# Kernel tuning notes

Hardware: AMD Instinct MI355X
Metric: run time of the kernel (lower is better)

The kernel has to match this reference:

```python
import jax, jax.numpy as jnp
from jax import lax
import numpy as np

L, G, C = 4, 2, 4  # num_blocks, num_sparsity_groups, num_sparsity_cardinals
IMAGE_MEAN = 0.5
SCALE = 2


def _wn(v, g):
    # weight_norm over dims (1,2,3), g per output channel
    n = jnp.sqrt(jnp.sum(v * v, axis=(1, 2, 3), keepdims=True))
    return (g.reshape(-1, 1, 1, 1) / n) * v


def _conv(x, w, b, pad):
    y = lax.conv_general_dilated(x, w, (1, 1), [(pad, pad), (pad, pad)],
                                 dimension_numbers=('NCHW', 'OIHW', 'NCHW'))
    return y + b[None, :, None, None]


def _dyn_conv(x, v, g, b, mw, mb):
    # sparsity-routed conv: per-sample expert mixture of kernels
    w = _wn(v, g)                                   # [G*out, in, k, k]
    B = x.shape[0]
    logits = x.mean((-1, -2)) @ mw.T + mb           # [B, G*C]
    s = jax.nn.softmax(logits.reshape(B, G, C), axis=1)
    wv = w.reshape(G, C, -1, *w.shape[1:])          # [G, C, D, in, k, k]
    wper = jnp.einsum('bgc,gcdikl->bcdikl', s, wv)
    wper = wper.reshape(B, -1, *w.shape[1:])        # [B, out, in, k, k]
    bper = jnp.einsum('bgc,gcd->bcd', s, b.reshape(G, C, -1)).reshape(B, -1)

    def per_sample(xi, wi, bi):
        yi = lax.conv_general_dilated(xi[None], wi, (1, 1), [(1, 1), (1, 1)],
                                      dimension_numbers=('NCHW', 'OIHW', 'NCHW'))[0]
        return yi + bi[:, None, None]

    return jax.vmap(per_sample)(x, wper, bper)


def _pixel_shuffle(x, r):
    B, Cc, H, W = x.shape
    x = x.reshape(B, Cc // (r * r), r, r, H, W)
    x = x.transpose(0, 1, 4, 2, 5, 3)
    return x.reshape(B, Cc // (r * r), H * r, W * r)


def setup_inputs() -> dict:
    key = jax.random.key(0)
    ks = jax.random.split(key, 16)
    f32 = jnp.float32
    inp = {
        'x': jax.random.uniform(ks[0], (8, 3, 64, 64), dtype=f32),
        'head_v': jax.random.normal(ks[1], (64, 3, 3, 3), dtype=f32) * 0.05,
        'head_g': jnp.ones((64,), f32),
        'head_b': jnp.zeros((64,), f32),
        'b1_v': jax.random.normal(ks[2], (L, 512, 64, 3, 3), dtype=f32) * 0.05,
        'b1_g': jnp.full((L, 512), 2.0, f32),
        'b1_b': jnp.zeros((L, 512), f32),
        'b1_mw': jax.random.normal(ks[3], (L, 8, 64), dtype=f32) * 0.05,
        'b1_mb': jax.random.normal(ks[4], (L, 8), dtype=f32) * 0.05,
        'b2_v': jax.random.normal(ks[5], (L, 128, 256, 3, 3), dtype=f32) * 0.05,
        'b2_g': jnp.full((L, 128), 1.0 / np.sqrt(L), f32),
        'b2_b': jnp.zeros((L, 128), f32),
        'b2_mw': jax.random.normal(ks[6], (L, 8, 256), dtype=f32) * 0.05,
        'b2_mb': jax.random.normal(ks[7], (L, 8), dtype=f32) * 0.05,
        'tail_v': jax.random.normal(ks[8], (12, 64, 3, 3), dtype=f32) * 0.05,
        'tail_g': jnp.ones((12,), f32),
        'tail_b': jnp.zeros((12,), f32),
        'skip_v': jax.random.normal(ks[9], (12, 3, 5, 5), dtype=f32) * 0.05,
        'skip_g': jnp.ones((12,), f32),
        'skip_b': jnp.zeros((12,), f32),
    }
    return inp


def reference(x, head_v, head_g, head_b,
              b1_v, b1_g, b1_b, b1_mw, b1_mb,
              b2_v, b2_g, b2_b, b2_mw, b2_mb,
              tail_v, tail_g, tail_b,
              skip_v, skip_g, skip_b):
    x = x - IMAGE_MEAN
    h = _conv(x, _wn(head_v, head_g), head_b, pad=1)
    for l in range(L):
        r0 = h
        t = _dyn_conv(h, b1_v[l], b1_g[l], b1_b[l], b1_mw[l], b1_mb[l])
        t = jax.nn.relu(t)
        t = _dyn_conv(t, b2_v[l], b2_g[l], b2_b[l], b2_mw[l], b2_mb[l])
        h = t + r0
    body = _conv(h, _wn(tail_v, tail_g), tail_b, pad=1)
    s = _conv(x, _wn(skip_v, skip_g), skip_b, pad=2)
    y = _pixel_shuffle(body + s, SCALE) + IMAGE_MEAN
    return y
```

## Files before the change

kernel.cpp:

```cpp
#include <hip/hip_runtime.h>

typedef __attribute__((ext_vector_type(8))) short bf16x8;
typedef __attribute__((ext_vector_type(4))) float f32x4;
typedef __attribute__((ext_vector_type(8))) unsigned short u16x8;

__device__ __forceinline__ unsigned short bf16u(float x) {
    unsigned int u = __builtin_bit_cast(unsigned int, x);
    unsigned int r = (u + 0x7fffu + ((u >> 16) & 1u)) >> 16;
    return (unsigned short)r;
}
__device__ __forceinline__ float bf2f(unsigned short u) {
    return __builtin_bit_cast(float, (unsigned int)u << 16);
}
__device__ __forceinline__ void gll16(const void* g, void* l) {
    __builtin_amdgcn_global_load_lds((const __attribute__((address_space(1))) void*)g,
                                     (__attribute__((address_space(3))) void*)l, 16, 0, 0);
}

__global__ __launch_bounds__(256) void setup_kernel(
    unsigned short* __restrict__ hbf, unsigned short* __restrict__ tbf,
    float* __restrict__ sums,
    const float* __restrict__ hv, const float* __restrict__ hg, float* __restrict__ hw,
    const float* __restrict__ kv, const float* __restrict__ kg, float* __restrict__ kw) {
    int blk = blockIdx.x;
    if (blk < 335) {
        int i = blk * 256 + threadIdx.x;
        u16x8 z8 = {0, 0, 0, 0, 0, 0, 0, 0};
        if (i < 16640) {
            int chv = i & 3, pb = i >> 2, pos = pb % 260, bc = pb / 260;
            int y, x;
            if (pos < 66) { y = 0; x = pos; }
            else if (pos < 132) { y = 65; x = pos - 66; }
            else if (pos < 196) { y = pos - 131; x = 0; }
            else { y = pos - 195; x = 65; }
            *(u16x8*)&hbf[((size_t)bc * 4356 + y * 66 + x) * 32 + chv * 8] = z8;
        } else if (i < 83200) {
            int j = i - 16640;
            int chv = j & 3, pb = j >> 2, pos = pb % 260, bc = pb / 260;
            int y, x;
            if (pos < 66) { y = 0; x = pos; }
            else if (pos < 132) { y = 65; x = pos - 66; }
            else if (pos < 196) { y = pos - 131; x = 0; }
            else { y = pos - 195; x = 65; }
            *(u16x8*)&tbf[((size_t)bc * 4356 + y * 66 + x) * 32 + chv * 8] = z8;
        } else {
            int k = i - 83200;
            f32x4 z4 = {0.f, 0.f, 0.f, 0.f};
            ((f32x4*)sums)[k] = z4;
        }
        return;
    }
    int b2 = blk - 335;
    const float *v, *g;
    float* outw;
    int len, row;
    if (b2 < 64) { v = hv; g = hg; outw = hw; len = 27; row = b2; }
    else         { v = kv; g = kg; outw = kw; len = 75; row = b2 - 64; }
    __shared__ float red[4];
    __shared__ float s_sc;
    const float* vr = v + (size_t)row * len;
    float ss = 0.f;
    for (int i = threadIdx.x; i < len; i += 256) { float a = vr[i]; ss += a * a; }
    for (int o = 32; o > 0; o >>= 1) ss += __shfl_down(ss, o);
    if ((threadIdx.x & 63) == 0) red[threadIdx.x >> 6] = ss;
    __syncthreads();
    if (threadIdx.x == 0) s_sc = g[row] / sqrtf(red[0] + red[1] + red[2] + red[3]);
    __syncthreads();
    float sc = s_sc;
    float* orow = outw + (size_t)row * len;
    for (int i = threadIdx.x; i < len; i += 256) orow[i] = vr[i] * sc;
}

__global__ __launch_bounds__(256) void tail_repack2(const float* __restrict__ tv,
                                                    const float* __restrict__ tg,
                                                    unsigned short* __restrict__ wq) {
    __shared__ float row[576];
    __shared__ float red[4];
    __shared__ float s_sc;
    int mo = blockIdx.x;
    int tid = threadIdx.x;
    if (mo < 12) {
        for (int i = tid; i < 576; i += 256) row[i] = tv[mo * 576 + i];
        __syncthreads();
        float ss = 0.f;
        for (int i = tid; i < 576; i += 256) { float a = row[i]; ss += a * a; }
        for (int o = 32; o > 0; o >>= 1) ss += __shfl_down(ss, o);
        if ((tid & 63) == 0) red[tid >> 6] = ss;
        __syncthreads();
        if (tid == 0) s_sc = tg[mo] / sqrtf(red[0] + red[1] + red[2] + red[3]);
        __syncthreads();
        float sc = s_sc;
        for (int ch = tid; ch < 72; ch += 256) {
            int kg = ch & 3, c2 = ch >> 2;
            int t = c2 % 9, kc = c2 / 9;
            u16x8 pk;
#pragma unroll
            for (int kj = 0; kj < 8; ++kj) {
                int ic = kc * 32 + kg * 8 + kj;
                pk[kj] = bf16u(row[ic * 9 + t] * sc);
            }
            *(u16x8*)&wq[(size_t)((kc * 9 + t) * 4 + kg) * 128 + mo * 8] = pk;
        }
    } else {
        u16x8 z = {0, 0, 0, 0, 0, 0, 0, 0};
        for (int ch = tid; ch < 72; ch += 256) {
            int kg = ch & 3, c2 = ch >> 2;
            int t = c2 % 9, kc = c2 / 9;
            *(u16x8*)&wq[(size_t)((kc * 9 + t) * 4 + kg) * 128 + mo * 8] = z;
        }
    }
}

template <int IC, int GOC, int BPB, int LGMO>
__global__ __launch_bounds__(256) void combine_v3(
    const float* __restrict__ v, const float* __restrict__ g,
    const float* __restrict__ msum, const float* __restrict__ mw,
    const float* __restrict__ mb, float* __restrict__ s_out,
    unsigned short* __restrict__ wq, int D, int OC) {
    constexpr int ROWF = IC * 9;
    constexpr int KCh = IC / 32;
    constexpr int ROWS2 = 2 * GOC;
    constexpr int TOTC = GOC * KCh * 9 * 4;
    __shared__ float lv[ROWS2 * ROWF];
    __shared__ float lg[BPB][8];
    __shared__ float sv[BPB][8];
    __shared__ float scr[ROWS2];
    __shared__ float sw[BPB][ROWS2];
    int tid = threadIdx.x;
    int ocg = blockIdx.x * GOC;
    int b0 = blockIdx.y * BPB;
    for (int i = tid; i < ROWS2 * ROWF; i += 256) {
        int r = i / ROWF, jj = i - r * ROWF;
        int oc_r = (r / GOC) * OC + ocg + (r % GOC);
        lv[i] = v[(size_t)oc_r * ROWF + jj];
    }
    {
        int j = tid >> 5, l32 = tid & 31;
        for (int bb = 0; bb < BPB; ++bb) {
            float part = 0.f;
            for (int i = l32; i < IC; i += 32) part += msum[(b0 + bb) * IC + i] * mw[j * IC + i];
            for (int m = 16; m > 0; m >>= 1) part += __shfl_xor(part, m);
            if (l32 == 0) lg[bb][j] = part * (1.f / 4096.f) + mb[j];
        }
    }
    __syncthreads();
    {
        constexpr int TPR = 256 / ROWS2;
        int r = tid / TPR, lr = tid % TPR;
        float ss = 0.f;
        for (int i = lr; i < ROWF; i += TPR) { float a = lv[r * ROWF + i]; ss += a * a; }
#pragma unroll
        for (int m = (TPR > 32 ? 32 : TPR / 2); m > 0; m >>= 1) ss += __shfl_xor(ss, m);
        if (lr == 0) {
            int oc_r = (r / GOC) * OC + ocg + (r % GOC);
            scr[r] = g[oc_r] / sqrtf(ss);
        }
    }
    if (tid < BPB * 8) {
        int bb = tid >> 3, j = tid & 7;
        int gg = j >> 2, c = j & 3;
        float l0 = lg[bb][c], l1 = lg[bb][4 + c];
        float m = fmaxf(l0, l1);
        float e0 = __expf(l0 - m), e1 = __expf(l1 - m);
        float val = ((gg == 0) ? e0 : e1) / (e0 + e1);
        sv[bb][j] = val;
        if (blockIdx.x == 0) s_out[(b0 + bb) * 8 + j] = val;
    }
    __syncthreads();
    if (tid < BPB * ROWS2) {
        int bb = tid / ROWS2, r = tid % ROWS2;
        int oc = ocg + (r % GOC);
        int cd = oc / D;
        float s = (r < GOC) ? sv[bb][cd] : sv[bb][4 + cd];
        sw[bb][r] = s * scr[r];
    }
    __syncthreads();
    for (int ci = tid; ci < TOTC; ci += 256) {
        int ml = ci % GOC;
        int c = ci / GOC;
        int kg = c & 3, c2 = c >> 2;
        int t = c2 % 9, kc = c2 / 9;
        int oc = ocg + ml;
        const float* p0 = &lv[(size_t)ml * ROWF];
        const float* p1 = &lv[(size_t)(GOC + ml) * ROWF];
        float a0[8], a1[8];
#pragma unroll
        for (int kj = 0; kj < 8; ++kj) {
            int ic9 = (kc * 32 + kg * 8 + kj) * 9 + t;
            a0[kj] = p0[ic9];
            a1[kj] = p1[ic9];
        }
        for (int bb = 0; bb < BPB; ++bb) {
            float s0 = sw[bb][ml], s1 = sw[bb][GOC + ml];
            u16x8 pk;
#pragma unroll
            for (int kj = 0; kj < 8; ++kj) pk[kj] = bf16u(s0 * a0[kj] + s1 * a1[kj]);
            int b = b0 + bb;
            size_t w_off = ((((size_t)(b * (OC >> LGMO) + (oc >> LGMO)) * KCh + kc) * 9 + t) * 4 + kg)
                               * ((1 << LGMO) * 8) + (size_t)(oc & ((1 << LGMO) - 1)) * 8;
            *(u16x8*)&wq[w_off] = pk;
        }
    }
}

template <int IC, int OC, int MT, int WM, int WN, int NR,
          bool RELU, bool RES, bool WF32, bool WBF, int OCR, bool DYNB, int MINW>
__global__ __launch_bounds__(WM * WN * 64, MINW)
void conv_mfma(
    const unsigned short* __restrict__ in_bf,
    const unsigned short* __restrict__ wq,
    const float* __restrict__ bias_raw, const float* __restrict__ s8, int lgD,
    float* __restrict__ out,
    unsigned short* __restrict__ out_bf, float* __restrict__ msum, long wstride) {
    constexpr int THREADS = WM * WN * 64;
    constexpr int KCH = IC / 32;
    constexpr int NRH = NR + 2;
    constexpr int NT = NR * 64;
    constexpr int NF = (NT / 16) / WN;
    constexpr int MW = MT / (16 * WM);
    constexpr int WELEM = 9 * 32 * MT;
    constexpr int SELEM = NRH * 66 * 32;
    constexpr int SCH = SELEM / 8;
    constexpr int OCB = OCR / 32;

    __shared__ __align__(16) unsigned short S[2][SELEM];
    __shared__ float MRED[WN][MT];

    const int b = blockIdx.x, ot = blockIdx.z;
    const int y0 = blockIdx.y * NR;
    const int tid = threadIdx.x;
    const int lane = tid & 63;
    const int wid = tid >> 6;
    const int wm = wid / WN, wn = wid % WN;
    const int l15 = lane & 15, lk = lane >> 4;
    const int wmo = wm * (MT / WM);
    const int wno = wn * (NT / WN);

    f32x4 acc[MW][NF];
#pragma unroll
    for (int mf = 0; mf < MW; ++mf)
#pragma unroll
        for (int nf = 0; nf < NF; ++nf)
#pragma unroll
            for (int q = 0; q < 4; ++q) acc[mf][nf][q] = 0.f;

    const unsigned short* inb = in_bf + (size_t)b * KCH * (4356 * 32);
    const unsigned short* wqb = wq + (size_t)b * wstride + (size_t)ot * (KCH * WELEM);
    const unsigned short* wqa = wqb + (size_t)lk * (MT * 8) + (size_t)(wmo + l15) * 8;

    auto STAGE_S = [&](int kc, int buf) {
        const unsigned short* sb = inb + (size_t)kc * (4356 * 32);
        for (int i = tid; i < SCH; i += THREADS) {
            int Lz = i ^ ((i >> 3) & 7);
            int lk2 = Lz & 3, cr = Lz >> 2;
            int col = cr % 66, row = cr / 66;
            gll16(sb + ((size_t)(y0 + row) * 66 + col) * 32 + lk2 * 8,
                  (char*)S[buf] + i * 16);
        }
    };

    bf16x8 aT[2][MW];
#pragma unroll
    for (int mf = 0; mf < MW; ++mf) {
        aT[0][mf] = *(const bf16x8*)(wqa + mf * 128);
        aT[1][mf] = *(const bf16x8*)(wqa + (4 * MT * 8) + mf * 128);
    }
    STAGE_S(0, 0);
    __syncthreads();
#pragma unroll
    for (int kc = 0; kc < KCH; ++kc) {
        if (kc + 1 < KCH) STAGE_S(kc + 1, (kc + 1) & 1);
        const unsigned short* Sb = S[kc & 1];
#pragma unroll
        for (int t = 0; t < 9; ++t) {
            const int gt = kc * 9 + t;
            const int pp = gt & 1;
            const int dy = t / 3, dx = t % 3;
#pragma unroll
            for (int nf = 0; nf < NF; ++nf) {
                int n = wno + nf * 16 + l15;
                int r = n >> 6, c = n & 63;
                int L = ((r + dy) * 66 + (c + dx)) * 4 + lk;
                int P = L ^ ((L >> 3) & 7);
                bf16x8 bv = *(const bf16x8*)((const char*)Sb + P * 16);
#pragma unroll
                for (int mf = 0; mf < MW; ++mf)
                    acc[mf][nf] = __builtin_amdgcn_mfma_f32_16x16x32_bf16(aT[pp][mf], bv, acc[mf][nf], 0, 0, 0);
            }
            if (gt + 2 < KCH * 9) {
                const int ngt = gt + 2;
                const int nkc = ngt / 9, nt2 = ngt % 9;
#pragma unroll
                for (int mf = 0; mf < MW; ++mf)
                    aT[pp][mf] = *(const bf16x8*)(wqa + (size_t)nkc * WELEM + nt2 * (4 * MT * 8) + mf * 128);
            }
        }
        __syncthreads();
    }

    if constexpr (WBF) {
        static_assert(NF == 2, "shuffle epilogue needs NF==2");
        const int mynf = lk & 1;
        const int ch = lk >> 1;
        const bool evenlk = ((lk & 1) == 0);
#pragma unroll
        for (int mf = 0; mf < MW; ++mf) {
            int ocb = ot * MT + wmo + mf * 16 + lk * 4;
            float bvv[4];
#pragma unroll
            for (int q = 0; q < 4; ++q) {
                int oc = ocb + q;
                if (DYNB) {
                    int cc = oc >> lgD;
                    bvv[q] = s8[b * 8 + cc] * bias_raw[oc] + s8[b * 8 + 4 + cc] * bias_raw[OCR + oc];
                } else {
                    bvv[q] = bias_raw[oc];
                }
            }
            float r[2][4], pr[2][4];
#pragma unroll
            for (int nf = 0; nf < 2; ++nf)
#pragma unroll
                for (int q = 0; q < 4; ++q) {
                    float v = acc[mf][nf][q] + bvv[q];
                    if (RELU) v = fmaxf(v, 0.f);
                    r[nf][q] = v;
                }
#pragma unroll
            for (int nf = 0; nf < 2; ++nf)
#pragma unroll
                for (int q = 0; q < 4; ++q) pr[nf][q] = __shfl_xor(r[nf][q], 16);
            float v8[8];
#pragma unroll
            for (int q = 0; q < 4; ++q) {
                float a = r[mynf][q], p = pr[mynf][q];
                v8[q] = evenlk ? a : p;
                v8[4 + q] = evenlk ? p : a;
            }
            int n = wno + mynf * 16 + l15;
            int y = y0 + (n >> 6), x = n & 63;
            int occ = ot * MT + wmo + mf * 16 + ch * 8;
            size_t addr = ((((size_t)b * OCB + (occ >> 5)) * 66 + (y + 1)) * 66 + (x + 1)) * 32
                          + (occ & 31);
            if (RES) {
                u16x8 rv = *(const u16x8*)&out_bf[addr];
#pragma unroll
                for (int j = 0; j < 8; ++j) v8[j] += bf2f(rv[j]);
            }
            u16x8 pk;
#pragma unroll
            for (int j = 0; j < 8; ++j) pk[j] = bf16u(v8[j]);
            *(u16x8*)&out_bf[addr] = pk;
            if (msum) {
#pragma unroll
                for (int j = 0; j < 8; ++j) {
                    float t = v8[j];
                    t += __shfl_xor(t, 1);
                    t += __shfl_xor(t, 2);
                    t += __shfl_xor(t, 4);
                    t += __shfl_xor(t, 8);
                    t += __shfl_xor(t, 16);
                    v8[j] = t;
                }
                if ((lane & 31) == 0) {
#pragma unroll
                    for (int j = 0; j < 8; ++j)
                        MRED[wn][wmo + mf * 16 + ch * 8 + j] = v8[j];
                }
            }
        }
        if (msum) {
            __syncthreads();
            if (tid < MT) {
                float tot = 0.f;
#pragma unroll
                for (int w2 = 0; w2 < WN; ++w2) tot += MRED[w2][tid];
                atomicAdd(&msum[b * OCR + ot * MT + tid], tot);
            }
        }
    }
    if constexpr (WF32) {
#pragma unroll
        for (int mf = 0; mf < MW; ++mf) {
            int ocb = ot * MT + wmo + mf * 16 + lk * 4;
#pragma unroll
            for (int nf = 0; nf < NF; ++nf) {
                int n = wno + nf * 16 + l15;
                int y = y0 + (n >> 6), x = n & 63;
#pragma unroll
                for (int q = 0; q < 4; ++q) {
                    int oc = ocb + q;
                    if (oc < OCR) {
                        float v = acc[mf][nf][q] + bias_raw[oc];
                        out[(((size_t)b * OCR + oc) * 64 + y) * 64 + x] = v;
                    }
                }
            }
        }
    }
}

__global__ __launch_bounds__(256) void head_conv(
    const float* __restrict__ in, const float* __restrict__ w,
    const float* __restrict__ bias,
    unsigned short* __restrict__ out_bf, float* __restrict__ hsum0) {
    constexpr int OCT = 16, IC = 3;
    __shared__ float s_in[34 * 34];
    __shared__ float s_w[OCT * 9];
    __shared__ float wred[4][OCT];
    int b = blockIdx.z;
    int ocBase = blockIdx.y * OCT;
    int ty0 = (blockIdx.x >> 1) * 32;
    int tx0 = (blockIdx.x & 1) * 32;
    int tid = threadIdx.x;
    int lane = tid & 63, wid = tid >> 6;
    int tx = tid & 15, ty = tid >> 4;

    float acc[OCT][4];
#pragma unroll
    for (int oc = 0; oc < OCT; ++oc)
#pragma unroll
        for (int p = 0; p < 4; ++p) acc[oc][p] = 0.f;

    const float* inb = in + (size_t)b * IC * 4096;
    for (int ic = 0; ic < IC; ++ic) {
        const float* src = inb + (size_t)ic * 4096;
        for (int i = tid; i < 34 * 34; i += 256) {
            int r = i / 34, cc = i % 34;
            int gy = ty0 + r - 1, gx = tx0 + cc - 1;
            float val = 0.f;
            if (gy >= 0 && gy < 64 && gx >= 0 && gx < 64) val = src[gy * 64 + gx] - 0.5f;
            s_in[i] = val;
        }
        for (int i = tid; i < OCT * 9; i += 256) {
            int oc = i / 9, t = i % 9;
            s_w[i] = w[((size_t)(ocBase + oc) * IC + ic) * 9 + t];
        }
        __syncthreads();
        float v[4][4];
#pragma unroll
        for (int r = 0; r < 4; ++r)
#pragma unroll
            for (int cc = 0; cc < 4; ++cc) v[r][cc] = s_in[(2 * ty + r) * 34 + (2 * tx + cc)];
#pragma unroll
        for (int oc = 0; oc < OCT; ++oc) {
#pragma unroll
            for (int ky = 0; ky < 3; ++ky)
#pragma unroll
                for (int kx = 0; kx < 3; ++kx) {
                    float wv = s_w[oc * 9 + ky * 3 + kx];
                    acc[oc][0] += wv * v[ky][kx];
                    acc[oc][1] += wv * v[ky][kx + 1];
                    acc[oc][2] += wv * v[ky + 1][kx];
                    acc[oc][3] += wv * v[ky + 1][kx + 1];
                }
        }
        __syncthreads();
    }
    int py = ty0 + 2 * ty, px = tx0 + 2 * tx;
#pragma unroll
    for (int oc = 0; oc < OCT; ++oc) {
        int og = ocBase + oc;
        float bv = bias[og];
        float osum = 0.f;
#pragma unroll
        for (int p = 0; p < 4; ++p) {
            int dy = p >> 1, dx = p & 1;
            float val = acc[oc][p] + bv;
            osum += val;
            out_bf[((size_t)(b * 2 + (og >> 5)) * 4356 + (py + dy + 1) * 66 + (px + dx + 1)) * 32
                   + (og & 31)] = bf16u(val);
        }
        for (int m = 1; m < 64; m <<= 1) osum += __shfl_xor(osum, m);
        if (lane == 0) wred[wid][oc] = osum;
    }
    __syncthreads();
    if (tid < OCT)
        atomicAdd(&hsum0[b * 64 + ocBase + tid],
                  wred[0][tid] + wred[1][tid] + wred[2][tid] + wred[3][tid]);
}

__global__ __launch_bounds__(256) void shuffle_skip(
    const float* __restrict__ body, const float* __restrict__ x,
    const float* __restrict__ skw, const float* __restrict__ skb,
    float* __restrict__ out) {
    __shared__ float w[900];
    __shared__ float bb[12];
    int tid = threadIdx.x;
    for (int i = tid; i < 900; i += 256) w[i] = skw[i];
    if (tid < 12) bb[tid] = skb[tid];
    __syncthreads();
    int idx = blockIdx.x * 256 + tid;
    int ox = idx & 127;
    int oy = (idx >> 7) & 127;
    int v = idx >> 14;
    int c = v % 3;
    int b = v / 3;
    int rx = ox & 1, ry = oy & 1;
    int xx = ox >> 1, yy = oy >> 1;
    int ch = c * 4 + ry * 2 + rx;
    float acc = bb[ch];
    for (int ic = 0; ic < 3; ++ic)
        for (int ky = 0; ky < 5; ++ky) {
            int gy = yy + ky - 2;
            if (gy < 0 || gy >= 64) continue;
            for (int kx = 0; kx < 5; ++kx) {
                int gx = xx + kx - 2;
                if (gx < 0 || gx >= 64) continue;
                acc += w[((ch * 3 + ic) * 5 + ky) * 5 + kx] *
                       (x[((size_t)(b * 3 + ic) * 64 + gy) * 64 + gx] - 0.5f);
            }
        }
    size_t src = (((size_t)b * 12 + ch) * 64 + yy) * 64 + xx;
    out[idx] = body[src] + acc + 0.5f;
}

extern "C" void kernel_launch(void* const* d_in, const int* in_sizes, int n_in,
                              void* d_out, int out_size, void* d_ws, size_t ws_size,
                              hipStream_t stream) {
    const float* x      = (const float*)d_in[0];
    const float* head_v = (const float*)d_in[1];
    const float* head_g = (const float*)d_in[2];
    const float* head_b = (const float*)d_in[3];
    const float* b1_v   = (const float*)d_in[4];
    const float* b1_g   = (const float*)d_in[5];
    const float* b1_b   = (const float*)d_in[6];
    const float* b1_mw  = (const float*)d_in[7];
    const float* b1_mb  = (const float*)d_in[8];
    const float* b2_v   = (const float*)d_in[9];
    const float* b2_g   = (const float*)d_in[10];
    const float* b2_b   = (const float*)d_in[11];
    const float* b2_mw  = (const float*)d_in[12];
    const float* b2_mb  = (const float*)d_in[13];
    const float* tail_v = (const float*)d_in[14];
    const float* tail_g = (const float*)d_in[15];
    const float* tail_b = (const float*)d_in[16];
    const float* skip_v = (const float*)d_in[17];
    const float* skip_g = (const float*)d_in[18];
    const float* skip_b = (const float*)d_in[19];

    float* ws = (float*)d_ws;
    size_t off = 0;
    auto alloc = [&](size_t n) { float* p = ws + off; off += (n + 3) & ~(size_t)3; return p; };
    float* head_w = alloc(64 * 27);
    float* skip_w = alloc(12 * 75);
    float* sums   = alloc(10240);
    float* sbuf   = alloc(64);
    float* body   = alloc((size_t)8 * 12 * 4096);
    unsigned short* wq1  = (unsigned short*)alloc((size_t)8 * 256 * 576 / 2);
    unsigned short* wq2  = (unsigned short*)alloc((size_t)8 * 64 * 2304 / 2);
    unsigned short* wqt  = (unsigned short*)alloc(9216 / 2);
    unsigned short* h_bf = (unsigned short*)alloc((size_t)8 * 2 * 4356 * 32 / 2);
    unsigned short* t_bf = (unsigned short*)alloc((size_t)8 * 8 * 4356 * 32 / 2);
    (void)ws_size; (void)in_sizes; (void)n_in; (void)out_size;

    auto hsum = [&](int l) { return sums + l * 512; };
    auto tsum = [&](int l) { return sums + 2048 + l * 2048; };

    setup_kernel<<<411, 256, 0, stream>>>(h_bf, t_bf, sums, head_v, head_g, head_w,
                                          skip_v, skip_g, skip_w);
    tail_repack2<<<16, 256, 0, stream>>>(tail_v, tail_g, wqt);
    head_conv<<<dim3(4, 4, 8), 256, 0, stream>>>(x, head_w, head_b, h_bf, hsum(0));

    for (int l = 0; l < 4; ++l) {
        combine_v3<64, 4, 4, 5><<<dim3(64, 2), 256, 0, stream>>>(
            b1_v + (size_t)l * 512 * 576, b1_g + (size_t)l * 512, hsum(l),
            b1_mw + (size_t)l * 8 * 64, b1_mb + l * 8, sbuf, wq1, 64, 256);
        conv_mfma<64, 256, 32, 1, 4, 2, true, false, false, true, 256, true, 4>
            <<<dim3(8, 32, 8), 256, 0, stream>>>(h_bf, wq1, b1_b + (size_t)l * 512, sbuf, 6,
                                                 nullptr, t_bf, tsum(l), 147456);
        combine_v3<256, 2, 4, 6><<<dim3(32, 2), 256, 0, stream>>>(
            b2_v + (size_t)l * 128 * 2304, b2_g + (size_t)l * 128, tsum(l),
            b2_mw + (size_t)l * 8 * 256, b2_mb + l * 8, sbuf, wq2, 16, 64);
        conv_mfma<256, 64, 64, 4, 2, 1, false, true, false, true, 64, true, 4>
            <<<dim3(8, 64, 1), 512, 0, stream>>>(t_bf, wq2, b2_b + (size_t)l * 128, sbuf, 4,
                                                 nullptr, h_bf, (l < 3) ? hsum(l + 1) : nullptr,
                                                 147456);
    }

    conv_mfma<64, 16, 16, 1, 4, 4, false, false, true, false, 12, false, 2>
        <<<dim3(8, 16, 1), 256, 0, stream>>>(h_bf, wqt, tail_b, nullptr, 0,
                                             body, nullptr, nullptr, 0);
    shuffle_skip<<<1536, 256, 0, stream>>>(body, x, skip_w, skip_b, (float*)d_out);
}
```

Measured before the change: 338.1 us.

## Fuse skip conv and pixel shuffle into tail conv, retile dynamic convs

```diff
diff --git a/kernel.cpp b/kernel.cpp
--- a/kernel.cpp
+++ b/kernel.cpp
@@ -111,8 +111,8 @@
     }
 }
 
-template <int IC, int GOC, int BPB, int LGMO>
-__global__ __launch_bounds__(256) void combine_v3(
+template <int IC, int GOC, int LGMO>
+__global__ __launch_bounds__(256) void combine_v4(
     const float* __restrict__ v, const float* __restrict__ g,
     const float* __restrict__ msum, const float* __restrict__ mw,
     const float* __restrict__ mb, float* __restrict__ s_out,
@@ -121,14 +121,12 @@
     constexpr int KCh = IC / 32;
     constexpr int ROWS2 = 2 * GOC;
     constexpr int TOTC = GOC * KCh * 9 * 4;
+    constexpr int TPR = 256 / ROWS2;
     __shared__ float lv[ROWS2 * ROWF];
-    __shared__ float lg[BPB][8];
-    __shared__ float sv[BPB][8];
-    __shared__ float scr[ROWS2];
-    __shared__ float sw[BPB][ROWS2];
+    __shared__ float lg[8], sv8[8], scr[ROWS2], sw[ROWS2];
     int tid = threadIdx.x;
     int ocg = blockIdx.x * GOC;
-    int b0 = blockIdx.y * BPB;
+    int b = blockIdx.y;
     for (int i = tid; i < ROWS2 * ROWF; i += 256) {
         int r = i / ROWF, jj = i - r * ROWF;
         int oc_r = (r / GOC) * OC + ocg + (r % GOC);
@@ -136,43 +134,39 @@
     }
     {
         int j = tid >> 5, l32 = tid & 31;
-        for (int bb = 0; bb < BPB; ++bb) {
-            float part = 0.f;
-            for (int i = l32; i < IC; i += 32) part += msum[(b0 + bb) * IC + i] * mw[j * IC + i];
-            for (int m = 16; m > 0; m >>= 1) part += __shfl_xor(part, m);
-            if (l32 == 0) lg[bb][j] = part * (1.f / 4096.f) + mb[j];
-        }
+        float part = 0.f;
+        for (int i = l32; i < IC; i += 32) part += msum[b * IC + i] * mw[j * IC + i];
+        for (int m = 16; m > 0; m >>= 1) part += __shfl_xor(part, m);
+        if (l32 == 0) lg[j] = part * (1.f / 4096.f) + mb[j];
     }
     __syncthreads();
     {
-        constexpr int TPR = 256 / ROWS2;
         int r = tid / TPR, lr = tid % TPR;
         float ss = 0.f;
         for (int i = lr; i < ROWF; i += TPR) { float a = lv[r * ROWF + i]; ss += a * a; }
 #pragma unroll
-        for (int m = (TPR > 32 ? 32 : TPR / 2); m > 0; m >>= 1) ss += __shfl_xor(ss, m);
+        for (int m = TPR >> 1; m > 0; m >>= 1) ss += __shfl_xor(ss, m);
         if (lr == 0) {
             int oc_r = (r / GOC) * OC + ocg + (r % GOC);
             scr[r] = g[oc_r] / sqrtf(ss);
         }
     }
-    if (tid < BPB * 8) {
-        int bb = tid >> 3, j = tid & 7;
-        int gg = j >> 2, c = j & 3;
-        float l0 = lg[bb][c], l1 = lg[bb][4 + c];
+    if (tid < 8) {
+        int gg = tid >> 2, c = tid & 3;
+        float l0 = lg[c], l1 = lg[4 + c];
         float m = fmaxf(l0, l1);
         float e0 = __expf(l0 - m), e1 = __expf(l1 - m);
         float val = ((gg == 0) ? e0 : e1) / (e0 + e1);
-        sv[bb][j] = val;
-        if (blockIdx.x == 0) s_out[(b0 + bb) * 8 + j] = val;
-    }
-    __syncthreads();
-    if (tid < BPB * ROWS2) {
-        int bb = tid / ROWS2, r = tid % ROWS2;
+        sv8[tid] = val;
+        if (blockIdx.x == 0) s_out[b * 8 + tid] = val;
+    }
+    __syncthreads();
+    if (tid < ROWS2) {
+        int r = tid;
         int oc = ocg + (r % GOC);
         int cd = oc / D;
-        float s = (r < GOC) ? sv[bb][cd] : sv[bb][4 + cd];
-        sw[bb][r] = s * scr[r];
+        float s = (r < GOC) ? sv8[cd] : sv8[4 + cd];
+        sw[r] = s * scr[r];
     }
     __syncthreads();
     for (int ci = tid; ci < TOTC; ci += 256) {
@@ -181,37 +175,31 @@
         int kg = c & 3, c2 = c >> 2;
         int t = c2 % 9, kc = c2 / 9;
         int oc = ocg + ml;
+        float s0 = sw[ml], s1 = sw[GOC + ml];
         const float* p0 = &lv[(size_t)ml * ROWF];
         const float* p1 = &lv[(size_t)(GOC + ml) * ROWF];
-        float a0[8], a1[8];
+        u16x8 pk;
 #pragma unroll
         for (int kj = 0; kj < 8; ++kj) {
             int ic9 = (kc * 32 + kg * 8 + kj) * 9 + t;
-            a0[kj] = p0[ic9];
-            a1[kj] = p1[ic9];
-        }
-        for (int bb = 0; bb < BPB; ++bb) {
-            float s0 = sw[bb][ml], s1 = sw[bb][GOC + ml];
-            u16x8 pk;
-#pragma unroll
-            for (int kj = 0; kj < 8; ++kj) pk[kj] = bf16u(s0 * a0[kj] + s1 * a1[kj]);
-            int b = b0 + bb;
-            size_t w_off = ((((size_t)(b * (OC >> LGMO) + (oc >> LGMO)) * KCh + kc) * 9 + t) * 4 + kg)
-                               * ((1 << LGMO) * 8) + (size_t)(oc & ((1 << LGMO) - 1)) * 8;
-            *(u16x8*)&wq[w_off] = pk;
-        }
+            pk[kj] = bf16u(s0 * p0[ic9] + s1 * p1[ic9]);
+        }
+        size_t w_off = ((((size_t)(b * (OC >> LGMO) + (oc >> LGMO)) * KCh + kc) * 9 + t) * 4 + kg)
+                           * ((1 << LGMO) * 8) + (size_t)(oc & ((1 << LGMO) - 1)) * 8;
+        *(u16x8*)&wq[w_off] = pk;
     }
 }
 
 template <int IC, int OC, int MT, int WM, int WN, int NR,
-          bool RELU, bool RES, bool WF32, bool WBF, int OCR, bool DYNB, int MINW>
+          bool RELU, bool RES, bool WBF, bool TAILSH, int OCR, bool DYNB, int MINW>
 __global__ __launch_bounds__(WM * WN * 64, MINW)
 void conv_mfma(
     const unsigned short* __restrict__ in_bf,
     const unsigned short* __restrict__ wq,
     const float* __restrict__ bias_raw, const float* __restrict__ s8, int lgD,
-    float* __restrict__ out,
-    unsigned short* __restrict__ out_bf, float* __restrict__ msum, long wstride) {
+    unsigned short* __restrict__ out_bf, float* __restrict__ msum, long wstride,
+    float* __restrict__ dout, const float* __restrict__ xin,
+    const float* __restrict__ skw, const float* __restrict__ skb) {
     constexpr int THREADS = WM * WN * 64;
     constexpr int KCH = IC / 32;
     constexpr int NRH = NR + 2;
@@ -225,6 +213,8 @@
 
     __shared__ __align__(16) unsigned short S[2][SELEM];
     __shared__ float MRED[WN][MT];
+    __shared__ float SKW[TAILSH ? 912 : 1];
+    __shared__ float SKB[TAILSH ? 12 : 1];
 
     const int b = blockIdx.x, ot = blockIdx.z;
     const int y0 = blockIdx.y * NR;
@@ -236,6 +226,11 @@
     const int wmo = wm * (MT / WM);
     const int wno = wn * (NT / WN);
 
+    if constexpr (TAILSH) {
+        for (int i = tid; i < 900; i += THREADS) SKW[i] = skw[i];
+        if (tid < 12) SKB[tid] = skb[tid];
+    }
+
     f32x4 acc[MW][NF];
 #pragma unroll
     for (int mf = 0; mf < MW; ++mf)
@@ -262,8 +257,8 @@
     bf16x8 aT[2][MW];
 #pragma unroll
     for (int mf = 0; mf < MW; ++mf) {
-        aT[0][mf] = *(const bf16x8*)(wqa + mf * 128);
-        aT[1][mf] = *(const bf16x8*)(wqa + (4 * MT * 8) + mf * 128);
+        aT[0][mf] = *(const bf16x8*)(wqa + mf * (16 * 8));
+        aT[1][mf] = *(const bf16x8*)(wqa + (4 * MT * 8) + mf * (16 * 8));
     }
     STAGE_S(0, 0);
     __syncthreads();
@@ -292,17 +287,15 @@
                 const int nkc = ngt / 9, nt2 = ngt % 9;
 #pragma unroll
                 for (int mf = 0; mf < MW; ++mf)
-                    aT[pp][mf] = *(const bf16x8*)(wqa + (size_t)nkc * WELEM + nt2 * (4 * MT * 8) + mf * 128);
+                    aT[pp][mf] = *(const bf16x8*)(wqa + (size_t)nkc * WELEM + nt2 * (4 * MT * 8) + mf * (16 * 8));
             }
         }
         __syncthreads();
     }
 
     if constexpr (WBF) {
-        static_assert(NF == 2, "shuffle epilogue needs NF==2");
-        const int mynf = lk & 1;
         const int ch = lk >> 1;
-        const bool evenlk = ((lk & 1) == 0);
+        const bool oddlk = (lk & 1);
 #pragma unroll
         for (int mf = 0; mf < MW; ++mf) {
             int ocb = ot * MT + wmo + mf * 16 + lk * 4;
@@ -317,55 +310,65 @@
                     bvv[q] = bias_raw[oc];
                 }
             }
-            float r[2][4], pr[2][4];
-#pragma unroll
-            for (int nf = 0; nf < 2; ++nf)
+            int occ = ot * MT + wmo + mf * 16 + ch * 8;
+            float msr8[8];
+#pragma unroll
+            for (int j = 0; j < 8; ++j) msr8[j] = 0.f;
+#pragma unroll
+            for (int nfp = 0; nfp < NF; nfp += 2) {
+                float r0[2][4], pr[2][4];
+#pragma unroll
+                for (int h = 0; h < 2; ++h)
+#pragma unroll
+                    for (int q = 0; q < 4; ++q) {
+                        float v = acc[mf][nfp + h][q] + bvv[q];
+                        if (RELU) v = fmaxf(v, 0.f);
+                        r0[h][q] = v;
+                    }
+#pragma unroll
+                for (int h = 0; h < 2; ++h)
+#pragma unroll
+                    for (int q = 0; q < 4; ++q) pr[h][q] = __shfl_xor(r0[h][q], 16);
+                float v8[8];
 #pragma unroll
                 for (int q = 0; q < 4; ++q) {
-                    float v = acc[mf][nf][q] + bvv[q];
-                    if (RELU) v = fmaxf(v, 0.f);
-                    r[nf][q] = v;
-                }
-#pragma unroll
-            for (int nf = 0; nf < 2; ++nf)
-#pragma unroll
-                for (int q = 0; q < 4; ++q) pr[nf][q] = __shfl_xor(r[nf][q], 16);
-            float v8[8];
-#pragma unroll
-            for (int q = 0; q < 4; ++q) {
-                float a = r[mynf][q], p = pr[mynf][q];
-                v8[q] = evenlk ? a : p;
-                v8[4 + q] = evenlk ? p : a;
-            }
-            int n = wno + mynf * 16 + l15;
-            int y = y0 + (n >> 6), x = n & 63;
-            int occ = ot * MT + wmo + mf * 16 + ch * 8;
-            size_t addr = ((((size_t)b * OCB + (occ >> 5)) * 66 + (y + 1)) * 66 + (x + 1)) * 32
-                          + (occ & 31);
-            if (RES) {
-                u16x8 rv = *(const u16x8*)&out_bf[addr];
-#pragma unroll
-                for (int j = 0; j < 8; ++j) v8[j] += bf2f(rv[j]);
-            }
-            u16x8 pk;
-#pragma unroll
-            for (int j = 0; j < 8; ++j) pk[j] = bf16u(v8[j]);
-            *(u16x8*)&out_bf[addr] = pk;
+                    float own = oddlk ? r0[1][q] : r0[0][q];
+                    float oth = oddlk ? pr[1][q] : pr[0][q];
+                    v8[q]     = oddlk ? oth : own;
+                    v8[4 + q] = oddlk ? own : oth;
+                }
+                int mynf = nfp + (lk & 1);
+                int n = wno + mynf * 16 + l15;
+                int y = y0 + (n >> 6), x = n & 63;
+                size_t addr = ((((size_t)b * OCB + (occ >> 5)) * 66 + (y + 1)) * 66 + (x + 1)) * 32
+                              + (occ & 31);
+                if (RES) {
+                    u16x8 rv = *(const u16x8*)&out_bf[addr];
+#pragma unroll
+                    for (int j = 0; j < 8; ++j) v8[j] += bf2f(rv[j]);
+                }
+                u16x8 pk;
+#pragma unroll
+                for (int j = 0; j < 8; ++j) pk[j] = bf16u(v8[j]);
+                *(u16x8*)&out_bf[addr] = pk;
+#pragma unroll
+                for (int j = 0; j < 8; ++j) msr8[j] += v8[j];
+            }
             if (msum) {
 #pragma unroll
                 for (int j = 0; j < 8; ++j) {
-                    float t = v8[j];
+                    float t = msr8[j];
                     t += __shfl_xor(t, 1);
                     t += __shfl_xor(t, 2);
                     t += __shfl_xor(t, 4);
                     t += __shfl_xor(t, 8);
                     t += __shfl_xor(t, 16);
-                    v8[j] = t;
+                    msr8[j] = t;
                 }
                 if ((lane & 31) == 0) {
 #pragma unroll
                     for (int j = 0; j < 8; ++j)
-                        MRED[wn][wmo + mf * 16 + ch * 8 + j] = v8[j];
+                        MRED[wn][wmo + mf * 16 + ch * 8 + j] = msr8[j];
                 }
             }
         }
@@ -379,21 +382,33 @@
             }
         }
     }
-    if constexpr (WF32) {
-#pragma unroll
-        for (int mf = 0; mf < MW; ++mf) {
-            int ocb = ot * MT + wmo + mf * 16 + lk * 4;
-#pragma unroll
-            for (int nf = 0; nf < NF; ++nf) {
-                int n = wno + nf * 16 + l15;
-                int y = y0 + (n >> 6), x = n & 63;
-#pragma unroll
-                for (int q = 0; q < 4; ++q) {
-                    int oc = ocb + q;
-                    if (oc < OCR) {
-                        float v = acc[mf][nf][q] + bias_raw[oc];
-                        out[(((size_t)b * OCR + oc) * 64 + y) * 64 + x] = v;
+    if constexpr (TAILSH) {
+#pragma unroll
+        for (int nf = 0; nf < NF; ++nf) {
+            int n = wno + nf * 16 + l15;
+            int y = y0 + (n >> 6), x = n & 63;
+#pragma unroll
+            for (int q = 0; q < 4; ++q) {
+                int oc = lk * 4 + q;
+                if (oc < 12) {
+                    float vv = acc[0][nf][q] + bias_raw[oc];
+                    float sk = SKB[oc];
+                    for (int ic = 0; ic < 3; ++ic) {
+                        const float* xb = xin + ((size_t)(b * 3 + ic) << 12);
+                        for (int ky = 0; ky < 5; ++ky) {
+                            int gy = y + ky - 2;
+                            if (gy < 0 || gy >= 64) continue;
+                            for (int kx = 0; kx < 5; ++kx) {
+                                int gx = x + kx - 2;
+                                if (gx < 0 || gx >= 64) continue;
+                                sk += SKW[((oc * 3 + ic) * 5 + ky) * 5 + kx] *
+                                      (xb[gy * 64 + gx] - 0.5f);
+                            }
+                        }
                     }
+                    int c = oc >> 2, ry = (oc >> 1) & 1, rx = oc & 1;
+                    dout[((size_t)(b * 3 + c) * 128 + (2 * y + ry)) * 128 + (2 * x + rx)] =
+                        vv + sk + 0.5f;
                 }
             }
         }
@@ -478,41 +493,6 @@
     if (tid < OCT)
         atomicAdd(&hsum0[b * 64 + ocBase + tid],
                   wred[0][tid] + wred[1][tid] + wred[2][tid] + wred[3][tid]);
-}
-
-__global__ __launch_bounds__(256) void shuffle_skip(
-    const float* __restrict__ body, const float* __restrict__ x,
-    const float* __restrict__ skw, const float* __restrict__ skb,
-    float* __restrict__ out) {
-    __shared__ float w[900];
-    __shared__ float bb[12];
-    int tid = threadIdx.x;
-    for (int i = tid; i < 900; i += 256) w[i] = skw[i];
-    if (tid < 12) bb[tid] = skb[tid];
-    __syncthreads();
-    int idx = blockIdx.x * 256 + tid;
-    int ox = idx & 127;
-    int oy = (idx >> 7) & 127;
-    int v = idx >> 14;
-    int c = v % 3;
-    int b = v / 3;
-    int rx = ox & 1, ry = oy & 1;
-    int xx = ox >> 1, yy = oy >> 1;
-    int ch = c * 4 + ry * 2 + rx;
-    float acc = bb[ch];
-    for (int ic = 0; ic < 3; ++ic)
-        for (int ky = 0; ky < 5; ++ky) {
-            int gy = yy + ky - 2;
-            if (gy < 0 || gy >= 64) continue;
-            for (int kx = 0; kx < 5; ++kx) {
-                int gx = xx + kx - 2;
-                if (gx < 0 || gx >= 64) continue;
-                acc += w[((ch * 3 + ic) * 5 + ky) * 5 + kx] *
-                       (x[((size_t)(b * 3 + ic) * 64 + gy) * 64 + gx] - 0.5f);
-            }
-        }
-    size_t src = (((size_t)b * 12 + ch) * 64 + yy) * 64 + xx;
-    out[idx] = body[src] + acc + 0.5f;
 }
 
 extern "C" void kernel_launch(void* const* d_in, const int* in_sizes, int n_in,
@@ -546,7 +526,6 @@
     float* skip_w = alloc(12 * 75);
     float* sums   = alloc(10240);
     float* sbuf   = alloc(64);
-    float* body   = alloc((size_t)8 * 12 * 4096);
     unsigned short* wq1  = (unsigned short*)alloc((size_t)8 * 256 * 576 / 2);
     unsigned short* wq2  = (unsigned short*)alloc((size_t)8 * 64 * 2304 / 2);
     unsigned short* wqt  = (unsigned short*)alloc(9216 / 2);
@@ -563,23 +542,24 @@
     head_conv<<<dim3(4, 4, 8), 256, 0, stream>>>(x, head_w, head_b, h_bf, hsum(0));
 
     for (int l = 0; l < 4; ++l) {
-        combine_v3<64, 4, 4, 5><<<dim3(64, 2), 256, 0, stream>>>(
+        combine_v4<64, 4, 6><<<dim3(64, 8), 256, 0, stream>>>(
             b1_v + (size_t)l * 512 * 576, b1_g + (size_t)l * 512, hsum(l),
             b1_mw + (size_t)l * 8 * 64, b1_mb + l * 8, sbuf, wq1, 64, 256);
-        conv_mfma<64, 256, 32, 1, 4, 2, true, false, false, true, 256, true, 4>
-            <<<dim3(8, 32, 8), 256, 0, stream>>>(h_bf, wq1, b1_b + (size_t)l * 512, sbuf, 6,
-                                                 nullptr, t_bf, tsum(l), 147456);
-        combine_v3<256, 2, 4, 6><<<dim3(32, 2), 256, 0, stream>>>(
+        conv_mfma<64, 256, 64, 2, 2, 2, true, false, true, false, 256, true, 4>
+            <<<dim3(8, 32, 4), 256, 0, stream>>>(h_bf, wq1, b1_b + (size_t)l * 512, sbuf, 6,
+                                                 t_bf, tsum(l), 147456,
+                                                 nullptr, nullptr, nullptr, nullptr);
+        combine_v4<256, 2, 6><<<dim3(32, 8), 256, 0, stream>>>(
             b2_v + (size_t)l * 128 * 2304, b2_g + (size_t)l * 128, tsum(l),
             b2_mw + (size_t)l * 8 * 256, b2_mb + l * 8, sbuf, wq2, 16, 64);
-        conv_mfma<256, 64, 64, 4, 2, 1, false, true, false, true, 64, true, 4>
-            <<<dim3(8, 64, 1), 512, 0, stream>>>(t_bf, wq2, b2_b + (size_t)l * 128, sbuf, 4,
-                                                 nullptr, h_bf, (l < 3) ? hsum(l + 1) : nullptr,
-                                                 147456);
-    }
-
-    conv_mfma<64, 16, 16, 1, 4, 4, false, false, true, false, 12, false, 2>
+        conv_mfma<256, 64, 64, 4, 2, 2, false, true, true, false, 64, true, 2>
+            <<<dim3(8, 32, 1), 512, 0, stream>>>(t_bf, wq2, b2_b + (size_t)l * 128, sbuf, 4,
+                                                 h_bf, (l < 3) ? hsum(l + 1) : nullptr, 147456,
+                                                 nullptr, nullptr, nullptr, nullptr);
+    }
+
+    conv_mfma<64, 16, 16, 1, 4, 4, false, false, false, true, 12, false, 2>
         <<<dim3(8, 16, 1), 256, 0, stream>>>(h_bf, wqt, tail_b, nullptr, 0,
-                                             body, nullptr, nullptr, 0);
-    shuffle_skip<<<1536, 256, 0, stream>>>(body, x, skip_w, skip_b, (float*)d_out);
-}
+                                             nullptr, nullptr, 0,
+                                             (float*)d_out, x, skip_w, skip_b);
+}
```

After: 383.7 us. 13.5% more time.
